# Performance work log

Measured on AMD Instinct MI355X. Metric: run time of the kernel, lower is better.

## Reference

```python
import jax, jax.numpy as jnp
import numpy as np

NFIELD = 40

def setup_inputs() -> dict:
    key = jax.random.key(0)
    ks = jax.random.split(key, 7)
    B, F, E, A = 1024, NFIELD, 128, 128
    s = 1.0 / np.sqrt(E)
    return {
        "x": jax.random.normal(ks[0], (B, F, E), dtype=jnp.float32),
        "attn_w_w": jax.random.normal(ks[1], (A, E), dtype=jnp.float32) * s,
        "attn_w_b": jax.random.normal(ks[2], (A,), dtype=jnp.float32) * s,
        "attn_h_w": jax.random.normal(ks[3], (1, A), dtype=jnp.float32) * s,
        "attn_h_b": jax.random.normal(ks[4], (1,), dtype=jnp.float32) * s,
        "attn_p_w": jax.random.normal(ks[5], (1, E), dtype=jnp.float32) * s,
        "attn_p_b": jax.random.normal(ks[6], (1,), dtype=jnp.float32) * s,
    }

def reference(x, attn_w_w, attn_w_b, attn_h_w, attn_h_b, attn_p_w, attn_p_b):
    # x: [B, F, E]; pairwise field interactions over upper-triangular (i<j) pairs
    nfield = x.shape[1]
    vi, vj = np.triu_indices(nfield, k=1)  # static index arrays, P = F*(F-1)/2
    hp = x[:, vi, :] * x[:, vj, :]                                   # [B, P, E]
    aw = jax.nn.relu(jnp.einsum('bpe,ae->bpa', hp, attn_w_w) + attn_w_b)  # [B, P, A]
    scores = jnp.einsum('bpa,oa->bpo', aw, attn_h_w) + attn_h_b          # [B, P, 1]
    attn = jax.nn.softmax(scores, axis=1)                                # softmax over pairs
    afm = jnp.sum(attn * hp, axis=1)                                     # [B, E]
    out = jnp.einsum('be,oe->bo', afm, attn_p_w) + attn_p_b              # [B, 1]
    return out.squeeze(1)                                                # [B]
```

## Files before the change

### kernel.cpp

```cpp
#include <hip/hip_runtime.h>

#define NF 40
#define NE 128
#define NA 128
#define NP 780
#define NPT 784
#define NMT 49
#define XS_LD 132

typedef short short8 __attribute__((ext_vector_type(8)));
typedef float floatx4 __attribute__((ext_vector_type(4)));

__device__ __forceinline__ unsigned cvt_pk_bf16(float lo, float hi) {
    unsigned r;
    asm("v_cvt_pk_bf16_f32 %0, %1, %2" : "=v"(r) : "v"(lo), "v"(hi));
    return r;
}

__device__ __forceinline__ float rowsum16(float x) {
    x += __int_as_float(__builtin_amdgcn_update_dpp(0, __float_as_int(x), 0x121, 0xf, 0xf, true));
    x += __int_as_float(__builtin_amdgcn_update_dpp(0, __float_as_int(x), 0x122, 0xf, 0xf, true));
    x += __int_as_float(__builtin_amdgcn_update_dpp(0, __float_as_int(x), 0x124, 0xf, 0xf, true));
    x += __int_as_float(__builtin_amdgcn_update_dpp(0, __float_as_int(x), 0x128, 0xf, 0xf, true));
    return x;
}

__global__ __launch_bounds__(256)
void afm_prep_kernel(const float* __restrict__ wg,
                     unsigned short* __restrict__ wbf,
                     int* __restrict__ ijg)
{
    const int t = blockIdx.x * 256 + threadIdx.x;
    if (t < NA * NE / 4) {
        float4 v = *(const float4*)(wg + t * 4);
        uint2 pk;
        pk.x = cvt_pk_bf16(v.x, v.y);
        pk.y = cvt_pk_bf16(v.z, v.w);
        *(uint2*)(wbf + t * 4) = pk;
    }
    if (t < NPT) {
        int v = 0;
        if (t < NP) {
            int i = 0, rem = t;
            while (rem >= (NF - 1 - i)) { rem -= (NF - 1 - i); ++i; }
            v = (i << 8) | (i + 1 + rem);
        }
        ijg[t] = v;
    }
}

__global__ __launch_bounds__(256, 2)
void afm_fused_kernel(const float* __restrict__ xg,
                      const unsigned short* __restrict__ wbf,
                      const int* __restrict__ ijg,
                      const float* __restrict__ wbg,
                      const float* __restrict__ hg,
                      const float* __restrict__ pwg,
                      const float* __restrict__ pbg,
                      float* __restrict__ out)
{
    __shared__ float xs[NF][XS_LD];
    __shared__ float sc[NPT];
    __shared__ int   ij[NPT];
    __shared__ float afmp[4][NE];
    __shared__ int   rs[NF + 1];
    __shared__ float red_max[4], red_sum[4], red_out[4];

    const int tid  = threadIdx.x;
    const int b    = blockIdx.x;
    const int lane = tid & 63;
    const int wid  = tid >> 6;
    const int col  = lane & 15;
    const int quad = (lane >> 4) & 3;

    const float* xb = xg + (size_t)b * (NF * NE);
    for (int t = tid; t < NF * (NE / 4); t += 256) {
        int row = t >> 5, c = (t & 31) * 4;
        float4 v = *(const float4*)(xb + row * NE + c);
        *(float4*)&xs[row][c] = v;
    }
    if (tid < NPT / 4) {
        *(int4*)&ij[tid * 4] = ((const int4*)ijg)[tid];
    }
    if (tid <= NF) {
        rs[tid] = tid * (2 * NF - 1 - tid) / 2;
    }
    float wbr[8], hr[8];
#pragma unroll
    for (int n = 0; n < 8; ++n) {
        wbr[n] = wbg[n * 16 + col];
        hr[n]  = hg[n * 16 + col];
    }
    short8 bfrag[8][4];
#pragma unroll
    for (int n = 0; n < 8; ++n)
#pragma unroll
        for (int k = 0; k < 4; ++k)
            bfrag[n][k] = *(const short8*)(wbf + (n * 16 + col) * NE + k * 32 + quad * 8);
    __syncthreads();

    for (int mt = wid; mt < NMT; mt += 4) {
        const int p0 = mt * 16;
        const int v  = ij[p0 + col];
        const float* xip = &xs[(v >> 8) & 255][0];
        const float* xjp = &xs[v & 255][0];

        floatx4 acc[8];
#pragma unroll
        for (int n = 0; n < 8; ++n)
            acc[n] = (floatx4){wbr[n], wbr[n], wbr[n], wbr[n]};

#pragma unroll
        for (int k = 0; k < 4; ++k) {
            const int koff = k * 32 + quad * 8;
            float4 i0 = *(const float4*)(xip + koff);
            float4 i1 = *(const float4*)(xip + koff + 4);
            float4 j0 = *(const float4*)(xjp + koff);
            float4 j1 = *(const float4*)(xjp + koff + 4);
            union { short8 s; unsigned u[4]; } af;
            af.u[0] = cvt_pk_bf16(i0.x * j0.x, i0.y * j0.y);
            af.u[1] = cvt_pk_bf16(i0.z * j0.z, i0.w * j0.w);
            af.u[2] = cvt_pk_bf16(i1.x * j1.x, i1.y * j1.y);
            af.u[3] = cvt_pk_bf16(i1.z * j1.z, i1.w * j1.w);
#pragma unroll
            for (int n = 0; n < 8; ++n)
                acc[n] = __builtin_amdgcn_mfma_f32_16x16x32_bf16(af.s, bfrag[n][k], acc[n], 0, 0, 0);
        }

        float ps[4] = {0.f, 0.f, 0.f, 0.f};
#pragma unroll
        for (int n = 0; n < 8; ++n) {
#pragma unroll
            for (int r = 0; r < 4; ++r)
                ps[r] += fmaxf(acc[n][r], 0.f) * hr[n];
        }
#pragma unroll
        for (int r = 0; r < 4; ++r) ps[r] = rowsum16(ps[r]);
        if (col == 0) {
#pragma unroll
            for (int r = 0; r < 4; ++r) {
                int p = p0 + quad * 4 + r;
                if (p < NP) sc[p] = ps[r];
            }
        }
    }
    __syncthreads();

    float m = -1e30f;
    for (int p = tid; p < NP; p += 256) m = fmaxf(m, sc[p]);
#pragma unroll
    for (int off = 1; off < 64; off <<= 1) m = fmaxf(m, __shfl_xor(m, off));
    if (lane == 0) red_max[wid] = m;
    __syncthreads();
    const float M = fmaxf(fmaxf(red_max[0], red_max[1]), fmaxf(red_max[2], red_max[3]));

    float s = 0.f;
    for (int p = tid; p < NP; p += 256) {
        float e = __expf(sc[p] - M);
        sc[p] = e;
        s += e;
    }
#pragma unroll
    for (int off = 1; off < 64; off <<= 1) s += __shfl_xor(s, off);
    if (lane == 0) red_sum[wid] = s;
    __syncthreads();

    {
        const int e2   = lane * 2;
        const int pbeg = wid * 195;
        const int pend = pbeg + 195;
        float a0 = 0.f, a1 = 0.f;
        int p = pbeg;
        int i = ij[pbeg] >> 8;
        while (p < pend) {
            int segend = rs[i + 1];
            int pe = segend < pend ? segend : pend;
            float2 vi = *(const float2*)&xs[i][e2];
            const float* xj = &xs[i + 1 + (p - rs[i])][e2];
            for (; p < pe; ++p) {
                float w = sc[p];
                float2 vj = *(const float2*)xj;
                a0 += w * vi.x * vj.x;
                a1 += w * vi.y * vj.y;
                xj += XS_LD;
            }
            ++i;
        }
        *(float2*)&afmp[wid][e2] = make_float2(a0, a1);
    }
    __syncthreads();

    float vv = 0.f;
    if (tid < NE) {
        float a = afmp[0][tid] + afmp[1][tid] + afmp[2][tid] + afmp[3][tid];
        vv = a * pwg[tid];
    }
#pragma unroll
    for (int off = 1; off < 64; off <<= 1) vv += __shfl_xor(vv, off);
    if (lane == 0) red_out[wid] = vv;
    __syncthreads();
    if (tid == 0) {
        float S   = red_sum[0] + red_sum[1] + red_sum[2] + red_sum[3];
        float tot = red_out[0] + red_out[1] + red_out[2] + red_out[3];
        out[b] = tot / S + pbg[0];
    }
}

extern "C" void kernel_launch(void* const* d_in, const int* in_sizes, int n_in,
                              void* d_out, int out_size, void* d_ws, size_t ws_size,
                              hipStream_t stream) {
    const float* xg  = (const float*)d_in[0];
    const float* wg  = (const float*)d_in[1];
    const float* wbg = (const float*)d_in[2];
    const float* hg  = (const float*)d_in[3];
    const float* pwg = (const float*)d_in[5];
    const float* pbg = (const float*)d_in[6];
    const int B = in_sizes[0] / (NF * NE);

    unsigned short* wbf = (unsigned short*)d_ws;
    int* ijg = (int*)((char*)d_ws + NA * NE * sizeof(unsigned short));

    afm_prep_kernel<<<16, 256, 0, stream>>>(wg, wbf, ijg);
    afm_fused_kernel<<<B, 256, 0, stream>>>(xg, wbf, ijg, wbg, hg, pwg, pbg, (float*)d_out);
}
```

Measured before the change: 136.1 us.

## Raise occupancy hint and vectorize pair-weighted sum via index table

Raises the launch-bounds minimum from 2 to 4 blocks per CU, which pushes the compiler to use fewer registers so more waves can be resident. It also replaces the segmented row-walk in the attention-weighted sum with a flat loop over padded pairs that reads four pair indices and four weights as vectors. Padded pairs get zero exp weight so they add nothing. The tighter register cap risks spilling, since each thread holds 32 B-fragment vectors (128 VGPRs) plus the accumulators, and the new loop reads both x_i and x_j rows from LDS for every pair.

New measurement: 279.2 us. +105.1%, slower.

```diff
diff --git a/kernel.cpp b/kernel.cpp
--- a/kernel.cpp
+++ b/kernel.cpp
@@ -49,7 +49,7 @@
     }
 }
 
-__global__ __launch_bounds__(256, 2)
+__global__ __launch_bounds__(256, 4)
 void afm_fused_kernel(const float* __restrict__ xg,
                       const unsigned short* __restrict__ wbf,
                       const int* __restrict__ ijg,
@@ -63,7 +63,6 @@
     __shared__ float sc[NPT];
     __shared__ int   ij[NPT];
     __shared__ float afmp[4][NE];
-    __shared__ int   rs[NF + 1];
     __shared__ float red_max[4], red_sum[4], red_out[4];
 
     const int tid  = threadIdx.x;
@@ -81,9 +80,6 @@
     }
     if (tid < NPT / 4) {
         *(int4*)&ij[tid * 4] = ((const int4*)ijg)[tid];
-    }
-    if (tid <= NF) {
-        rs[tid] = tid * (2 * NF - 1 - tid) / 2;
     }
     float wbr[8], hr[8];
 #pragma unroll
@@ -155,8 +151,8 @@
     const float M = fmaxf(fmaxf(red_max[0], red_max[1]), fmaxf(red_max[2], red_max[3]));
 
     float s = 0.f;
-    for (int p = tid; p < NP; p += 256) {
-        float e = __expf(sc[p] - M);
+    for (int p = tid; p < NPT; p += 256) {
+        float e = (p < NP) ? __expf(sc[p] - M) : 0.f;
         sc[p] = e;
         s += e;
     }
@@ -167,24 +163,23 @@
 
     {
         const int e2   = lane * 2;
-        const int pbeg = wid * 195;
-        const int pend = pbeg + 195;
+        const int pbeg = wid * 196;
         float a0 = 0.f, a1 = 0.f;
-        int p = pbeg;
-        int i = ij[pbeg] >> 8;
-        while (p < pend) {
-            int segend = rs[i + 1];
-            int pe = segend < pend ? segend : pend;
-            float2 vi = *(const float2*)&xs[i][e2];
-            const float* xj = &xs[i + 1 + (p - rs[i])][e2];
-            for (; p < pe; ++p) {
-                float w = sc[p];
-                float2 vj = *(const float2*)xj;
-                a0 += w * vi.x * vj.x;
-                a1 += w * vi.y * vj.y;
-                xj += XS_LD;
-            }
-            ++i;
+        for (int p = pbeg; p < pbeg + 196; p += 4) {
+            int4   v4 = *(const int4*)&ij[p];
+            float4 w4 = *(const float4*)&sc[p];
+            float2 i0 = *(const float2*)&xs[(v4.x >> 8) & 255][e2];
+            float2 j0 = *(const float2*)&xs[v4.x & 255][e2];
+            float2 i1 = *(const float2*)&xs[(v4.y >> 8) & 255][e2];
+            float2 j1 = *(const float2*)&xs[v4.y & 255][e2];
+            float2 i2 = *(const float2*)&xs[(v4.z >> 8) & 255][e2];
+            float2 j2 = *(const float2*)&xs[v4.z & 255][e2];
+            float2 i3 = *(const float2*)&xs[(v4.w >> 8) & 255][e2];
+            float2 j3 = *(const float2*)&xs[v4.w & 255][e2];
+            a0 += w4.x * i0.x * j0.x;  a1 += w4.x * i0.y * j0.y;
+            a0 += w4.y * i1.x * j1.x;  a1 += w4.y * i1.y * j1.y;
+            a0 += w4.z * i2.x * j2.x;  a1 += w4.z * i2.y * j2.y;
+            a0 += w4.w * i3.x * j3.x;  a1 += w4.w * i3.y * j3.y;
         }
         *(float2*)&afmp[wid][e2] = make_float2(a0, a1);
     }
```
